# Performance work log

Hardware: AMD Instinct MI355X
Metric: run time of the kernel (lower is better)

## Reference

```python
import jax, jax.numpy as jnp
import numpy as np

GAMMA = 1.0
INPUT_DIM = 512
NUM_CENTERS = 4096
BATCH = 16384


def setup_inputs() -> dict:
    key = jax.random.key(0)
    kx, kc = jax.random.split(key)
    x = jax.random.normal(kx, (BATCH, INPUT_DIM), dtype=jnp.float32)
    centers = jax.random.normal(kc, (NUM_CENTERS, INPUT_DIM), dtype=jnp.float32)
    return {"x": x, "centers": centers}


def reference(x, centers):
    x_sq = jnp.sum(x * x, axis=-1, keepdims=True)            # [B, 1]
    c_sq = jnp.sum(centers * centers, axis=-1)               # [C]
    cross = jnp.einsum("bd,cd->bc", x, centers)              # [B, C]
    dist_sq = x_sq - 2.0 * cross + c_sq[None, :]
    return jnp.exp(-GAMMA * dist_sq)
```

## Files before the change

kernel.cpp:

```cpp
#include <hip/hip_runtime.h>
#include <stdint.h>

#define M_DIM 16384
#define N_DIM 4096
#define K_DIM 512

typedef int v8i __attribute__((ext_vector_type(8)));
typedef float f32x16 __attribute__((ext_vector_type(16)));
typedef float f32x4v __attribute__((ext_vector_type(4)));

typedef __attribute__((address_space(3))) uint32_t lds_u32_t;
typedef const __attribute__((address_space(1))) uint32_t glob_u32_t;

__device__ __forceinline__ void gload16(const void* g, void* l) {
    __builtin_amdgcn_global_load_lds((glob_u32_t*)g, (lds_u32_t*)l, 16, 0, 0);
}

__global__ __launch_bounds__(256)
void convert_norm_kernel(const float* __restrict__ X, const float* __restrict__ C,
                         uint8_t* __restrict__ Apack, uint8_t* __restrict__ Bf8,
                         float* __restrict__ xsq, float* __restrict__ csq) {
    const int wave = threadIdx.x >> 6;
    const int lane = threadIdx.x & 63;
    const int row = blockIdx.x * 4 + wave;

    const float* src;
    uint8_t* dst;
    float* nrm;
    int r;
    size_t off;
    if (row < M_DIM) {
        src = X; dst = Apack; nrm = xsq; r = row;
        off = (size_t)((r >> 5) * 8 + (lane >> 3)) * 2048
            + ((lane >> 2) & 1) * 1024 + (r & 31) * 32 + (lane & 3) * 8;
    } else {
        src = C; dst = Bf8; nrm = csq; r = row - M_DIM;
        off = (size_t)r * K_DIM + lane * 8;
    }

    const float4* p = (const float4*)(src + (size_t)r * K_DIM) + lane * 2;
    float4 a = p[0], b = p[1];
    uint32_t lo = 0, hi = 0;
    lo = __builtin_amdgcn_cvt_pk_fp8_f32(a.x, a.y, lo, false);
    lo = __builtin_amdgcn_cvt_pk_fp8_f32(a.z, a.w, lo, true);
    hi = __builtin_amdgcn_cvt_pk_fp8_f32(b.x, b.y, hi, false);
    hi = __builtin_amdgcn_cvt_pk_fp8_f32(b.z, b.w, hi, true);
    *(uint2*)(dst + off) = make_uint2(lo, hi);

    float s = a.x*a.x + a.y*a.y + a.z*a.z + a.w*a.w
            + b.x*b.x + b.y*b.y + b.z*b.z + b.w*b.w;
    #pragma unroll
    for (int o2 = 32; o2 > 0; o2 >>= 1) s += __shfl_down(s, o2, 64);
    if (lane == 0) nrm[r] = s;
}

__global__ __launch_bounds__(256, 4)
void rbf_mfma_kernel(const uint8_t* __restrict__ Apack, const uint8_t* __restrict__ B8,
                     const float* __restrict__ xsq, const float* __restrict__ csq,
                     float* __restrict__ out) {
    __shared__ uint8_t Bs[128 * 128];

    const int tid = threadIdx.x;
    const int lv  = tid & 63;
    const int w   = tid >> 6;
    const int h   = lv >> 5;
    const int r31 = lv & 31;

    const int bn = (blockIdx.x & 31) * 128;
    const int bm = (blockIdx.x >> 5) * 128;

    const int tr = tid >> 3;
    const int tc = tid & 7;
    const int cc = (tc - tr) & 7;
    const uint8_t* gB = B8 + (size_t)(bn + 4 * tr) * K_DIM + cc * 16;
    uint8_t* BsW = Bs + w * 1024;

    const uint8_t* aB = Apack + (size_t)((bm >> 5) + w) * 16384 + h * 1024 + r31 * 32;

    const uint8_t* bRow = Bs + r31 * 128;

    f32x16 acc[4] = {};

    for (int kk = 0; kk < 4; ++kk) {
        const int koff = kk * 128;
        #pragma unroll
        for (int R = 0; R < 4; ++R)
            gload16(gB + koff + (size_t)R * K_DIM, BsW + R * 4096);

        uint4 a0[2], a1[2];
        #pragma unroll
        for (int ksl = 0; ksl < 2; ++ksl) {
            const uint8_t* ap = aB + (2 * kk + ksl) * 2048;
            a0[ksl] = *(const uint4*)(ap);
            a1[ksl] = *(const uint4*)(ap + 16);
        }
        __syncthreads();

        #pragma unroll
        for (int ksl = 0; ksl < 2; ++ksl) {
            v8i av = (v8i){(int)a0[ksl].x, (int)a0[ksl].y, (int)a0[ksl].z, (int)a0[ksl].w,
                           (int)a1[ksl].x, (int)a1[ksl].y, (int)a1[ksl].z, (int)a1[ksl].w};
            const int c0 = ksl * 4 + 2 * h;
            const int s0 = ((c0 + 0 + r31) & 7) * 16;
            const int s1 = ((c0 + 1 + r31) & 7) * 16;
            #pragma unroll
            for (int j = 0; j < 4; ++j) {
                uint4 lo = *(const uint4*)(bRow + j * 4096 + s0);
                uint4 hi = *(const uint4*)(bRow + j * 4096 + s1);
                v8i bv = (v8i){(int)lo.x, (int)lo.y, (int)lo.z, (int)lo.w,
                               (int)hi.x, (int)hi.y, (int)hi.z, (int)hi.w};
                acc[j] = __builtin_amdgcn_mfma_scale_f32_32x32x64_f8f6f4(
                    av, bv, acc[j],
                    0 , 0 ,
                    0, 0x7F7F7F7Fu, 0, 0x7F7F7F7Fu);
            }
        }
        if (kk < 3) __syncthreads();
    }

    const float4 cs4 = *(const float4*)(csq + bn + 4 * r31);
    const int mbase = bm + 32 * w + 4 * h;

    #pragma unroll
    for (int g = 0; g < 4; ++g) {
        const float4 xs4 = *(const float4*)(xsq + mbase + 8 * g);
        #pragma unroll
        for (int rr = 0; rr < 4; ++rr) {
            const int reg = g * 4 + rr;
            const float xs = (rr == 0) ? xs4.x : (rr == 1) ? xs4.y
                           : (rr == 2) ? xs4.z : xs4.w;
            const int gm = mbase + 8 * g + rr;
            f32x4v o;
            o.x = __expf(-(xs - 2.0f * acc[0][reg] + cs4.x));
            o.y = __expf(-(xs - 2.0f * acc[1][reg] + cs4.y));
            o.z = __expf(-(xs - 2.0f * acc[2][reg] + cs4.z));
            o.w = __expf(-(xs - 2.0f * acc[3][reg] + cs4.w));
            __builtin_nontemporal_store(
                o, (f32x4v*)(out + (size_t)gm * N_DIM + bn + 4 * r31));
        }
    }
}

extern "C" void kernel_launch(void* const* d_in, const int* in_sizes, int n_in,
                              void* d_out, int out_size, void* d_ws, size_t ws_size,
                              hipStream_t stream) {
    const float* X = (const float*)d_in[0];
    const float* C = (const float*)d_in[1];
    float* out = (float*)d_out;

    uint8_t* Apack = (uint8_t*)d_ws;
    uint8_t* Bf8 = Apack + (size_t)M_DIM * K_DIM;
    float* xsq = (float*)(Bf8 + (size_t)N_DIM * K_DIM);
    float* csq = xsq + M_DIM;

    convert_norm_kernel<<<(M_DIM + N_DIM) / 4, 256, 0, stream>>>(X, C, Apack, Bf8, xsq, csq);
    rbf_mfma_kernel<<<(M_DIM / 128) * (N_DIM / 128), 256, 0, stream>>>(Apack, Bf8, xsq, csq, out);
}
```

Measured before the change: 300.8 us.

## Prepack centers into MFMA fragment layout and load B directly from global

The convert kernel now writes the FP8 centers in a pre-swizzled fragment layout matching the MFMA operand order, so the GEMM kernel reads B straight from global memory into registers. This drops the LDS staging buffer, the global_load_lds path and all __syncthreads, and fully unrolls the K loop. Block indices are also remapped so consecutive blocks spread across M tiles for cache locality. Each wave now fetches B from global/L2 on its own rather than sharing one LDS copy across the block's four waves, which raises cache traffic.

```diff
diff --git a/kernel.cpp b/kernel.cpp
--- a/kernel.cpp
+++ b/kernel.cpp
@@ -9,16 +9,9 @@
 typedef float f32x16 __attribute__((ext_vector_type(16)));
 typedef float f32x4v __attribute__((ext_vector_type(4)));
 
-typedef __attribute__((address_space(3))) uint32_t lds_u32_t;
-typedef const __attribute__((address_space(1))) uint32_t glob_u32_t;
-
-__device__ __forceinline__ void gload16(const void* g, void* l) {
-    __builtin_amdgcn_global_load_lds((glob_u32_t*)g, (lds_u32_t*)l, 16, 0, 0);
-}
-
 __global__ __launch_bounds__(256)
 void convert_norm_kernel(const float* __restrict__ X, const float* __restrict__ C,
-                         uint8_t* __restrict__ Apack, uint8_t* __restrict__ Bf8,
+                         uint8_t* __restrict__ Apack, uint8_t* __restrict__ Bpack,
                          float* __restrict__ xsq, float* __restrict__ csq) {
     const int wave = threadIdx.x >> 6;
     const int lane = threadIdx.x & 63;
@@ -34,8 +27,13 @@
         off = (size_t)((r >> 5) * 8 + (lane >> 3)) * 2048
             + ((lane >> 2) & 1) * 1024 + (r & 31) * 32 + (lane & 3) * 8;
     } else {
-        src = C; dst = Bf8; nrm = csq; r = row - M_DIM;
-        off = (size_t)r * K_DIM + lane * 8;
+        src = C; dst = Bpack; nrm = csq; r = row - M_DIM;
+        off = (size_t)(r >> 7) * 65536
+            + (r & 3) * 16384
+            + (lane >> 3) * 2048
+            + ((lane >> 2) & 1) * 1024
+            + ((r & 127) >> 2) * 32
+            + (lane & 3) * 8;
     }
 
     const float4* p = (const float4*)(src + (size_t)r * K_DIM) + lane * 2;
@@ -55,67 +53,43 @@
 }
 
 __global__ __launch_bounds__(256, 4)
-void rbf_mfma_kernel(const uint8_t* __restrict__ Apack, const uint8_t* __restrict__ B8,
+void rbf_mfma_kernel(const uint8_t* __restrict__ Apack, const uint8_t* __restrict__ Bpack,
                      const float* __restrict__ xsq, const float* __restrict__ csq,
                      float* __restrict__ out) {
-    __shared__ uint8_t Bs[128 * 128];
-
     const int tid = threadIdx.x;
     const int lv  = tid & 63;
     const int w   = tid >> 6;
     const int h   = lv >> 5;
     const int r31 = lv & 31;
 
-    const int bn = (blockIdx.x & 31) * 128;
-    const int bm = (blockIdx.x >> 5) * 128;
-
-    const int tr = tid >> 3;
-    const int tc = tid & 7;
-    const int cc = (tc - tr) & 7;
-    const uint8_t* gB = B8 + (size_t)(bn + 4 * tr) * K_DIM + cc * 16;
-    uint8_t* BsW = Bs + w * 1024;
+    const int sw = (blockIdx.x & 7) * 512 + (blockIdx.x >> 3);
+    const int bn = (sw & 31) * 128;
+    const int bm = (sw >> 5) * 128;
 
     const uint8_t* aB = Apack + (size_t)((bm >> 5) + w) * 16384 + h * 1024 + r31 * 32;
-
-    const uint8_t* bRow = Bs + r31 * 128;
+    const uint8_t* bB = Bpack + (size_t)(bn >> 7) * 65536 + h * 1024 + r31 * 32;
 
     f32x16 acc[4] = {};
 
-    for (int kk = 0; kk < 4; ++kk) {
-        const int koff = kk * 128;
+    #pragma unroll
+    for (int ks = 0; ks < 8; ++ks) {
+        const uint8_t* ap = aB + ks * 2048;
+        const uint8_t* bp = bB + ks * 2048;
+        uint4 a0 = *(const uint4*)(ap);
+        uint4 a1 = *(const uint4*)(ap + 16);
+        v8i av = (v8i){(int)a0.x, (int)a0.y, (int)a0.z, (int)a0.w,
+                       (int)a1.x, (int)a1.y, (int)a1.z, (int)a1.w};
         #pragma unroll
-        for (int R = 0; R < 4; ++R)
-            gload16(gB + koff + (size_t)R * K_DIM, BsW + R * 4096);
-
-        uint4 a0[2], a1[2];
-        #pragma unroll
-        for (int ksl = 0; ksl < 2; ++ksl) {
-            const uint8_t* ap = aB + (2 * kk + ksl) * 2048;
-            a0[ksl] = *(const uint4*)(ap);
-            a1[ksl] = *(const uint4*)(ap + 16);
+        for (int j = 0; j < 4; ++j) {
+            uint4 lo = *(const uint4*)(bp + j * 16384);
+            uint4 hi = *(const uint4*)(bp + j * 16384 + 16);
+            v8i bv = (v8i){(int)lo.x, (int)lo.y, (int)lo.z, (int)lo.w,
+                           (int)hi.x, (int)hi.y, (int)hi.z, (int)hi.w};
+            acc[j] = __builtin_amdgcn_mfma_scale_f32_32x32x64_f8f6f4(
+                av, bv, acc[j],
+                0 , 0 ,
+                0, 0x7F7F7F7Fu, 0, 0x7F7F7F7Fu);
         }
-        __syncthreads();
-
-        #pragma unroll
-        for (int ksl = 0; ksl < 2; ++ksl) {
-            v8i av = (v8i){(int)a0[ksl].x, (int)a0[ksl].y, (int)a0[ksl].z, (int)a0[ksl].w,
-                           (int)a1[ksl].x, (int)a1[ksl].y, (int)a1[ksl].z, (int)a1[ksl].w};
-            const int c0 = ksl * 4 + 2 * h;
-            const int s0 = ((c0 + 0 + r31) & 7) * 16;
-            const int s1 = ((c0 + 1 + r31) & 7) * 16;
-            #pragma unroll
-            for (int j = 0; j < 4; ++j) {
-                uint4 lo = *(const uint4*)(bRow + j * 4096 + s0);
-                uint4 hi = *(const uint4*)(bRow + j * 4096 + s1);
-                v8i bv = (v8i){(int)lo.x, (int)lo.y, (int)lo.z, (int)lo.w,
-                               (int)hi.x, (int)hi.y, (int)hi.z, (int)hi.w};
-                acc[j] = __builtin_amdgcn_mfma_scale_f32_32x32x64_f8f6f4(
-                    av, bv, acc[j],
-                    0 , 0 ,
-                    0, 0x7F7F7F7Fu, 0, 0x7F7F7F7Fu);
-            }
-        }
-        if (kk < 3) __syncthreads();
     }
 
     const float4 cs4 = *(const float4*)(csq + bn + 4 * r31);
@@ -149,10 +123,10 @@
     float* out = (float*)d_out;
 
     uint8_t* Apack = (uint8_t*)d_ws;
-    uint8_t* Bf8 = Apack + (size_t)M_DIM * K_DIM;
-    float* xsq = (float*)(Bf8 + (size_t)N_DIM * K_DIM);
+    uint8_t* Bpack = Apack + (size_t)M_DIM * K_DIM;
+    float* xsq = (float*)(Bpack + (size_t)N_DIM * K_DIM);
     float* csq = xsq + M_DIM;
 
-    convert_norm_kernel<<<(M_DIM + N_DIM) / 4, 256, 0, stream>>>(X, C, Apack, Bf8, xsq, csq);
-    rbf_mfma_kernel<<<(M_DIM / 128) * (N_DIM / 128), 256, 0, stream>>>(Apack, Bf8, xsq, csq, out);
+    convert_norm_kernel<<<(M_DIM + N_DIM) / 4, 256, 0, stream>>>(X, C, Apack, Bpack, xsq, csq);
+    rbf_mfma_kernel<<<(M_DIM / 128) * (N_DIM / 128), 256, 0, stream>>>(Apack, Bpack, xsq, csq, out);
 }
```

After: 476.7 us. 1.58x slower.
